# Kernel tuning notes

Hardware: AMD Instinct MI355X
Metric: run time of the kernel (lower is better)

Reference implementation:

```python
import jax, jax.numpy as jnp
import numpy as np

N = 100000          # nodes
E = 1600000         # edges (avg degree 16)
D_IN = 128
D_OUT = 128
K = 3               # Chebyshev order
LAMBDA_MAX = 2.0    # PyG default for sym normalization


def setup_inputs() -> dict:
    key = jax.random.key(0)
    k1, k2, k3, k4 = jax.random.split(key, 4)
    x = jax.random.normal(k1, (N, D_IN), dtype=jnp.float32)
    edge_index = jax.random.randint(k2, (2, E), 0, N, dtype=jnp.int32)
    # Glorot-ish init for the K per-order linear weights
    weight = jax.random.normal(k3, (K, D_IN, D_OUT), dtype=jnp.float32) * (1.0 / np.sqrt(D_IN))
    bias = jax.random.normal(k4, (D_OUT,), dtype=jnp.float32) * 0.01
    return {"x": x, "edge_index": edge_index, "weight": weight, "bias": bias}


def reference(x, edge_index, weight, bias):
    src, dst = edge_index[0], edge_index[1]
    n = x.shape[0]

    # remove self loops (zero their weight), symmetric normalization
    ew = jnp.where(src != dst, 1.0, 0.0).astype(x.dtype)
    deg = jax.ops.segment_sum(ew, src, num_segments=n)
    dis = jnp.where(deg > 0, jax.lax.rsqrt(jnp.maximum(deg, 1.0)), 0.0)
    norm = dis[src] * ew * dis[dst]          # D^-1/2 A D^-1/2 entries

    # scaled Laplacian T-hat = (2/lmax) L - I, L = I - A_norm
    off_w = -(2.0 / LAMBDA_MAX) * norm       # off-diagonal entries
    diag_w = 2.0 / LAMBDA_MAX - 1.0          # = 0 for lambda_max=2

    def spmm(h):  # T-hat @ h : gather-multiply-scatter over edges
        agg = jax.ops.segment_sum(off_w[:, None] * h[src], dst, num_segments=n)
        return agg + diag_w * h

    # Chebyshev recurrence: Tx_k = 2 T-hat Tx_{k-1} - Tx_{k-2}
    Tx0 = x
    out = Tx0 @ weight[0]
    Tx1 = spmm(Tx0)
    out = out + Tx1 @ weight[1]
    for k in range(2, weight.shape[0]):
        Tx2 = 2.0 * spmm(Tx1) - Tx0
        out = out + Tx2 @ weight[k]
        Tx0, Tx1 = Tx1, Tx2
    return out + bias
```

## Files before the change

### kernel.cpp

```cpp
#include <hip/hip_runtime.h>
#include <hip/hip_bf16.h>

typedef __hip_bfloat16 bf16;
typedef __attribute__((ext_vector_type(8))) short short8;
typedef __attribute__((ext_vector_type(4))) float float4v;
typedef __attribute__((ext_vector_type(2))) float float2v;

#define N_NODES 100000
#define M_PAD   100096
#define N_EDGES 1600000
#define D 128
#define K_CAT 384
#define BUCKET_CAP 56
#define NBIN 392
#define BIN_CAP 4608
#define CHUNK 4096
#define NCHUNK 391
#define PREPB 192

__device__ __forceinline__ bf16 f2b(float v) { return __float2bfloat16(v); }
__device__ __forceinline__ float ub(unsigned int u, int k) {
    return (float)((u >> (k * 8)) & 0xffu);
}
__device__ __forceinline__ float2v cvt2lo(unsigned int u) {
    float a, b;
    asm("v_cvt_f32_ubyte0 %0, %2\n\t"
        "v_cvt_f32_ubyte1 %1, %2"
        : "=&v"(a), "=&v"(b) : "v"(u));
    float2v o; o.x = a; o.y = b; return o;
}
__device__ __forceinline__ float2v cvt2hi(unsigned int u) {
    float a, b;
    asm("v_cvt_f32_ubyte2 %0, %2\n\t"
        "v_cvt_f32_ubyte3 %1, %2"
        : "=&v"(a), "=&v"(b) : "v"(u));
    float2v o; o.x = a; o.y = b; return o;
}

__global__ __launch_bounds__(256) void phaseA_prep_kernel(const int* __restrict__ src,
                                                          const int* __restrict__ dst,
                                                          const float* __restrict__ w,
                                                          const float* __restrict__ bias,
                                                          int* __restrict__ gCursD,
                                                          int* __restrict__ gCursS,
                                                          unsigned int* __restrict__ gBinD,
                                                          unsigned char* __restrict__ gBinS,
                                                          bf16* __restrict__ wT,
                                                          float* __restrict__ biasf) {
    __shared__ int histD[NBIN], histS[NBIN], cursD[NBIN], cursS[NBIN];
    int tid = threadIdx.x;
    if (blockIdx.x >= NCHUNK) {
        int i = (blockIdx.x - NCHUNK) * 256 + tid;
        int o = i / K_CAT, k = i % K_CAT;
        float v;
        if (k < 128) {
            v = w[k * D + o] - w[2 * 16384 + k * D + o];
        } else if (k < 256) {
            v = w[16384 + (k - 128) * D + o];
        } else {
            v = 2.0f * w[2 * 16384 + (k - 256) * D + o];
        }
        wT[i] = f2b(v);
        if (i < D) biasf[i] = bias[i];
        return;
    }
    for (int t = tid; t < NBIN; t += 256) { histD[t] = 0; histS[t] = 0; }
    __syncthreads();
    int e0 = blockIdx.x * CHUNK;
    for (int i = tid; i < CHUNK; i += 256) {
        int e = e0 + i;
        if (e >= N_EDGES) break;
        int s = src[e], d = dst[e];
        if (s == d) continue;
        atomicAdd(&histD[d >> 8], 1);
        atomicAdd(&histS[s >> 8], 1);
    }
    __syncthreads();
    for (int t = tid; t < NBIN; t += 256) {
        cursD[t] = (histD[t] > 0) ? atomicAdd(&gCursD[t], histD[t]) : 0;
        cursS[t] = (histS[t] > 0) ? atomicAdd(&gCursS[t], histS[t]) : 0;
    }
    __syncthreads();
    for (int i = tid; i < CHUNK; i += 256) {
        int e = e0 + i;
        if (e >= N_EDGES) break;
        int s = src[e], d = dst[e];
        if (s == d) continue;
        int bd = d >> 8, bs = s >> 8;
        int sd = atomicAdd(&cursD[bd], 1);
        if (sd < BIN_CAP) gBinD[(size_t)bd * BIN_CAP + sd] = ((unsigned int)s << 8) | (unsigned int)(d & 255);
        int ss = atomicAdd(&cursS[bs], 1);
        if (ss < BIN_CAP) gBinS[(size_t)bs * BIN_CAP + ss] = (unsigned char)(s & 255);
    }
}

__global__ __launch_bounds__(256) void phaseBq_kernel(const int* __restrict__ gCursD,
                                                      const int* __restrict__ gCursS,
                                                      const unsigned int* __restrict__ gBinD,
                                                      const unsigned char* __restrict__ gBinS,
                                                      const float* __restrict__ x,
                                                      int* __restrict__ cnt,
                                                      float* __restrict__ dis,
                                                      int* __restrict__ bucket,
                                                      unsigned char* __restrict__ xq,
                                                      float* __restrict__ xscale,
                                                      float* __restrict__ dsx0) {
    __shared__ int curs[256];
    int tid = threadIdx.x;
    int b = blockIdx.x;
    curs[tid] = 0;
    __syncthreads();
    if (b < NBIN) {
        int count = min(gCursD[b], BIN_CAP);
        const unsigned int* rec = gBinD + (size_t)b * BIN_CAP;
        int n0 = b << 8;
        for (int j = tid; j < count; j += 256) {
            unsigned int r = rec[j];
            int dloc = r & 255;
            int s = (int)(r >> 8);
            int slot = atomicAdd(&curs[dloc], 1);
            if (slot < BUCKET_CAP) bucket[(size_t)(n0 + dloc) * BUCKET_CAP + slot] = s;
        }
        __syncthreads();
        int n = n0 + tid;
        if (n < N_NODES) cnt[n] = curs[tid];
    } else {
        int bb = b - NBIN;
        int count = min(gCursS[bb], BIN_CAP);
        const unsigned char* rec = gBinS + (size_t)bb * BIN_CAP;
        for (int j = tid; j < count; j += 256) {
            atomicAdd(&curs[rec[j]], 1);
        }
        __syncthreads();
        int n0 = bb << 8;
        int n = n0 + tid;
        if (n < N_NODES) {
            int c = curs[tid];
            dis[n] = (c > 0) ? rsqrtf((float)c) : 0.0f;
        }
        int wv = tid >> 6, lane = tid & 63;
        for (int i = 0; i < 64; i++) {
            int nn = n0 + wv * 64 + i;
            if (nn >= N_NODES) break;
            float2 v = *(const float2*)(x + (size_t)nn * D + lane * 2);
            float m = fmaxf(fabsf(v.x), fabsf(v.y));
#pragma unroll
            for (int k = 1; k < 64; k <<= 1) m = fmaxf(m, __shfl_xor(m, k));
            float inv = (m > 0.0f) ? 127.0f / m : 0.0f;
            int q0 = (int)rintf(v.x * inv) + 128;
            int q1 = (int)rintf(v.y * inv) + 128;
            *(unsigned short*)(xq + (size_t)nn * D + lane * 2) =
                (unsigned short)((q0 & 0xff) | ((q1 & 0xff) << 8));
            if (lane == 0) {
                float sc = m * (1.0f / 127.0f);
                int cc = curs[wv * 64 + i];
                float dnn = (cc > 0) ? rsqrtf((float)cc) : 0.0f;
                xscale[nn] = sc;
                dsx0[nn] = dnn * sc;
            }
        }
    }
}

template<int OUTQ>
__global__ __launch_bounds__(256) void spmm_q_kernel(const unsigned char* __restrict__ hq,
                                                     const float* __restrict__ dsx,
                                                     const float* __restrict__ dis,
                                                     const int* __restrict__ cnt,
                                                     const int* __restrict__ bucket,
                                                     unsigned char* __restrict__ outq,
                                                     float* __restrict__ oscale,
                                                     float* __restrict__ odsx,
                                                     bf16* __restrict__ outb) {
    int wv = threadIdx.x >> 6;
    int lane = threadIdx.x & 63;
    int n = blockIdx.x * 4 + wv;
    int c = min(cnt[n], BUCKET_CAP);
    float dn = dis[n];
    int q = lane >> 4;
    int r = lane & 15;
    int s_l = 0;
    float w_l = 0.0f;
    if (lane < c) {
        s_l = bucket[(size_t)n * BUCKET_CAP + lane];
        w_l = -dsx[s_l] * dn;
    }
    const unsigned char* hr = hq + (r << 3);

    float2v acc2[4];
#pragma unroll
    for (int k = 0; k < 4; k++) acc2[k] = (float2v)0.0f;
    float cw = 0.0f;

    int sA = __shfl(s_l, q), sB = __shfl(s_l, 4 + q);
    float wA = __shfl(w_l, q), wB = __shfl(w_l, 4 + q);
    uint2 uA = *(const uint2*)(hr + (size_t)sA * D);
    uint2 uB = *(const uint2*)(hr + (size_t)sB * D);

    for (int j0 = 0; j0 < c; j0 += 8) {
        int nj = j0 + 8;
        int sA2 = __shfl(s_l, nj + q);
        int sB2 = __shfl(s_l, nj + 4 + q);
        float wA2 = __shfl(w_l, nj + q);
        float wB2 = __shfl(w_l, nj + 4 + q);
        uint2 uA2 = *(const uint2*)(hr + (size_t)sA2 * D);
        uint2 uB2 = *(const uint2*)(hr + (size_t)sB2 * D);
        cw += wA + wB;
        float2v wAv; wAv.x = wA; wAv.y = wA;
        float2v wBv; wBv.x = wB; wBv.y = wB;
        acc2[0] += wAv * cvt2lo(uA.x);
        acc2[1] += wAv * cvt2hi(uA.x);
        acc2[2] += wAv * cvt2lo(uA.y);
        acc2[3] += wAv * cvt2hi(uA.y);
        acc2[0] += wBv * cvt2lo(uB.x);
        acc2[1] += wBv * cvt2hi(uB.x);
        acc2[2] += wBv * cvt2lo(uB.y);
        acc2[3] += wBv * cvt2hi(uB.y);
        sA = sA2; sB = sB2; wA = wA2; wB = wB2; uA = uA2; uB = uB2;
    }

    float acc[8];
#pragma unroll
    for (int k = 0; k < 4; k++) { acc[2 * k] = acc2[k].x; acc[2 * k + 1] = acc2[k].y; }
#pragma unroll
    for (int k = 0; k < 8; k++) {
        acc[k] += __shfl_xor(acc[k], 16);
        acc[k] += __shfl_xor(acc[k], 32);
    }
    cw += __shfl_xor(cw, 16);
    cw += __shfl_xor(cw, 32);
#pragma unroll
    for (int k = 0; k < 8; k++) acc[k] -= 128.0f * cw;

    if (OUTQ) {
        float m = 0.0f;
#pragma unroll
        for (int k = 0; k < 8; k++) m = fmaxf(m, fabsf(acc[k]));
#pragma unroll
        for (int k = 1; k < 16; k <<= 1) m = fmaxf(m, __shfl_xor(m, k));
        float inv = (m > 0.0f) ? 127.0f / m : 0.0f;
        if (q == 0) {
            unsigned int b0 = 0, b1 = 0;
#pragma unroll
            for (int k = 0; k < 4; k++)
                b0 |= ((unsigned int)((int)rintf(acc[k] * inv) + 128) & 0xffu) << (8 * k);
#pragma unroll
            for (int k = 0; k < 4; k++)
                b1 |= ((unsigned int)((int)rintf(acc[4 + k] * inv) + 128) & 0xffu) << (8 * k);
            uint2 pk; pk.x = b0; pk.y = b1;
            *(uint2*)(outq + (size_t)n * D + (r << 3)) = pk;
            if (lane == 0) {
                float sc = m * (1.0f / 127.0f);
                oscale[n] = sc;
                odsx[n] = dn * sc;
            }
        }
    } else {
        if (q == 0) {
            unsigned int p0 = (unsigned int)__bfloat16_as_ushort(f2b(acc[0])) |
                              ((unsigned int)__bfloat16_as_ushort(f2b(acc[1])) << 16);
            unsigned int p1 = (unsigned int)__bfloat16_as_ushort(f2b(acc[2])) |
                              ((unsigned int)__bfloat16_as_ushort(f2b(acc[3])) << 16);
            unsigned int p2 = (unsigned int)__bfloat16_as_ushort(f2b(acc[4])) |
                              ((unsigned int)__bfloat16_as_ushort(f2b(acc[5])) << 16);
            unsigned int p3 = (unsigned int)__bfloat16_as_ushort(f2b(acc[6])) |
                              ((unsigned int)__bfloat16_as_ushort(f2b(acc[7])) << 16);
            uint4 pk; pk.x = p0; pk.y = p1; pk.z = p2; pk.w = p3;
            *(uint4*)(outb + (size_t)n * D + (r << 3)) = pk;
        }
    }
}

#define AS_STRIDE 40
__device__ __forceinline__ void stage_q8(bf16* __restrict__ As,
                                         const unsigned char* __restrict__ srcq,
                                         const float* __restrict__ scl,
                                         int nb, int kb) {
    int tid = threadIdx.x;
#pragma unroll
    for (int t = 0; t < 2; t++) {
        int c = tid + t * 256;
        int row = c >> 2;
        int off = (c & 3) * 8;
        int gr = nb + row;
        if (gr > N_NODES - 1) gr = N_NODES - 1;
        uint2 u = *(const uint2*)(srcq + (size_t)gr * D + kb + off);
        float sc = scl[gr];
        float f0 = sc * (ub(u.x, 0) - 128.0f);
        float f1 = sc * (ub(u.x, 1) - 128.0f);
        float f2 = sc * (ub(u.x, 2) - 128.0f);
        float f3 = sc * (ub(u.x, 3) - 128.0f);
        float f4 = sc * (ub(u.y, 0) - 128.0f);
        float f5 = sc * (ub(u.y, 1) - 128.0f);
        float f6 = sc * (ub(u.y, 2) - 128.0f);
        float f7 = sc * (ub(u.y, 3) - 128.0f);
        uint4 pk;
        pk.x = (unsigned int)__bfloat16_as_ushort(f2b(f0)) |
               ((unsigned int)__bfloat16_as_ushort(f2b(f1)) << 16);
        pk.y = (unsigned int)__bfloat16_as_ushort(f2b(f2)) |
               ((unsigned int)__bfloat16_as_ushort(f2b(f3)) << 16);
        pk.z = (unsigned int)__bfloat16_as_ushort(f2b(f4)) |
               ((unsigned int)__bfloat16_as_ushort(f2b(f5)) << 16);
        pk.w = (unsigned int)__bfloat16_as_ushort(f2b(f6)) |
               ((unsigned int)__bfloat16_as_ushort(f2b(f7)) << 16);
        *(uint4*)(As + row * AS_STRIDE + off) = pk;
    }
}

__global__ __launch_bounds__(256) void gemm_kernel(const unsigned char* __restrict__ xq,
                                                   const float* __restrict__ xscale,
                                                   const unsigned char* __restrict__ tx1q,
                                                   const float* __restrict__ tx1scale,
                                                   const bf16* __restrict__ agg2,
                                                   const bf16* __restrict__ wT,
                                                   const float* __restrict__ biasf,
                                                   float* __restrict__ out) {
    __shared__ bf16 As[128 * AS_STRIDE];
    __shared__ bf16 Bs[128 * AS_STRIDE];

    int tid = threadIdx.x;
    int nb = blockIdx.x * 128;
    int w = tid >> 6;
    int lane = tid & 63;
    int lq = lane >> 4;
    int lr = lane & 15;

    float4v acc[2][8];
#pragma unroll
    for (int i = 0; i < 2; i++)
#pragma unroll
        for (int j = 0; j < 8; j++) acc[i][j] = (float4v)0.0f;

    for (int kc = 0; kc < 12; kc++) {
        int kbase = kc * 32;
        if (kc < 4) {
            stage_q8(As, xq, xscale, nb, kc * 32);
        } else if (kc < 8) {
            stage_q8(As, tx1q, tx1scale, nb, (kc - 4) * 32);
        } else {
            int soff = (kc & 3) * 32;
#pragma unroll
            for (int t = 0; t < 2; t++) {
                int c = tid + t * 256;
                int row = c >> 2;
                int off = (c & 3) * 8;
                uint4 v = *(const uint4*)(agg2 + (size_t)(nb + row) * D + soff + off);
                *(uint4*)(As + row * AS_STRIDE + off) = v;
            }
        }
#pragma unroll
        for (int t = 0; t < 2; t++) {
            int c = tid + t * 256;
            int row = c >> 2;
            int off = (c & 3) * 8;
            uint4 v = *(const uint4*)(wT + (size_t)row * K_CAT + kbase + off);
            *(uint4*)(Bs + row * AS_STRIDE + off) = v;
        }
        __syncthreads();

        short8 af[2], bfr[8];
#pragma unroll
        for (int i = 0; i < 2; i++)
            af[i] = *(const short8*)(As + (w * 32 + i * 16 + lr) * AS_STRIDE + lq * 8);
#pragma unroll
        for (int j = 0; j < 8; j++)
            bfr[j] = *(const short8*)(Bs + (j * 16 + lr) * AS_STRIDE + lq * 8);
#pragma unroll
        for (int i = 0; i < 2; i++)
#pragma unroll
            for (int j = 0; j < 8; j++)
                acc[i][j] = __builtin_amdgcn_mfma_f32_16x16x32_bf16(af[i], bfr[j], acc[i][j], 0, 0, 0);
        __syncthreads();
    }

#pragma unroll
    for (int i = 0; i < 2; i++) {
        int rowb = nb + w * 32 + i * 16 + lq * 4;
#pragma unroll
        for (int j = 0; j < 8; j++) {
            int col = j * 16 + lr;
            float bv = biasf[col];
#pragma unroll
            for (int r = 0; r < 4; r++) {
                int row = rowb + r;
                if (row < N_NODES) out[(size_t)row * D + col] = acc[i][j][r] + bv;
            }
        }
    }
}

extern "C" void kernel_launch(void* const* d_in, const int* in_sizes, int n_in,
                              void* d_out, int out_size, void* d_ws, size_t ws_size,
                              hipStream_t stream) {
    const float* x    = (const float*)d_in[0];
    const int*   ei   = (const int*)d_in[1];
    const float* w    = (const float*)d_in[2];
    const float* bias = (const float*)d_in[3];
    float* out = (float*)d_out;

    char* p = (char*)d_ws;
    int*   cnt      = (int*)p;     p += (size_t)N_NODES * 4;
    float* dis      = (float*)p;   p += (size_t)N_NODES * 4;
    int*   gCurs    = (int*)p;     p += (size_t)2 * NBIN * 4;
    float* dsx0     = (float*)p;   p += (size_t)M_PAD * 4;
    float* xscale   = (float*)p;   p += (size_t)M_PAD * 4;
    float* tx1scale = (float*)p;   p += (size_t)M_PAD * 4;
    float* dsx1     = (float*)p;   p += (size_t)M_PAD * 4;
    int*   bucket   = (int*)p;     p += (size_t)N_NODES * BUCKET_CAP * 4;
    char*  buf1     = p;           p += (size_t)M_PAD * D;
    unsigned char* xq = (unsigned char*)p; p += (size_t)M_PAD * D;
    bf16*  agg2     = (bf16*)p;    p += (size_t)M_PAD * D * 2;
    bf16*  wT       = (bf16*)p;    p += (size_t)D * K_CAT * 2;
    float* biasf    = (float*)p;   p += (size_t)D * 4;

    int*   gCursD = gCurs;
    int*   gCursS = gCurs + NBIN;
    unsigned int*  gBinD = (unsigned int*)buf1;
    unsigned char* gBinS = (unsigned char*)(gBinD + (size_t)NBIN * BIN_CAP);
    unsigned char* tx1q  = (unsigned char*)buf1;

    hipMemsetAsync(gCurs, 0, (size_t)2 * NBIN * 4, stream);

    phaseA_prep_kernel<<<NCHUNK + PREPB, 256, 0, stream>>>(ei, ei + N_EDGES, w, bias,
                                                           gCursD, gCursS, gBinD, gBinS,
                                                           wT, biasf);
    phaseBq_kernel<<<2 * NBIN, 256, 0, stream>>>(gCursD, gCursS, gBinD, gBinS, x,
                                                 cnt, dis, bucket, xq, xscale, dsx0);
    spmm_q_kernel<1><<<N_NODES / 4, 256, 0, stream>>>(xq, dsx0, dis, cnt, bucket,
                                                      tx1q, tx1scale, dsx1, (bf16*)nullptr);
    spmm_q_kernel<0><<<N_NODES / 4, 256, 0, stream>>>(tx1q, dsx1, dis, cnt, bucket,
                                                      (unsigned char*)nullptr, (float*)nullptr,
                                                      (float*)nullptr, agg2);
    gemm_kernel<<<M_PAD / 128, 256, 0, stream>>>(xq, xscale, tx1q, tx1scale,
                                                 agg2, wT, biasf, out);
}
```

Before: 353.4 us.

## Move x quantization into prep kernel and use persistent grid for SpMM

Quantizing x to int8 now happens in 25000 extra blocks of the first prep kernel, one wave per node. Before, it ran as a serial 64-node loop per wave inside the second half of phaseB, which had only 392 blocks. phaseB now only computes degrees and combines them with the precomputed scale. The SpMM kernels switch to a fixed grid of 2048 blocks that loop over node groups. This aims to raise parallelism in the quantization step and to cut block launch overhead in SpMM, at the cost of a much larger first grid and possible load imbalance across the grid-stride loop.

```diff
diff --git a/kernel.cpp b/kernel.cpp
--- a/kernel.cpp
+++ b/kernel.cpp
@@ -17,6 +17,8 @@
 #define CHUNK 4096
 #define NCHUNK 391
 #define PREPB 192
+#define QUANTB 25000
+#define SPMM_GRID 2048
 
 __device__ __forceinline__ bf16 f2b(float v) { return __float2bfloat16(v); }
 __device__ __forceinline__ float ub(unsigned int u, int k) {
@@ -37,18 +39,32 @@
     float2v o; o.x = a; o.y = b; return o;
 }
 
-__global__ __launch_bounds__(256) void phaseA_prep_kernel(const int* __restrict__ src,
-                                                          const int* __restrict__ dst,
-                                                          const float* __restrict__ w,
-                                                          const float* __restrict__ bias,
-                                                          int* __restrict__ gCursD,
-                                                          int* __restrict__ gCursS,
-                                                          unsigned int* __restrict__ gBinD,
-                                                          unsigned char* __restrict__ gBinS,
-                                                          bf16* __restrict__ wT,
-                                                          float* __restrict__ biasf) {
+__global__ __launch_bounds__(256) void phaseA_prep_quant_kernel(
+        const int* __restrict__ src, const int* __restrict__ dst,
+        const float* __restrict__ w, const float* __restrict__ bias,
+        const float* __restrict__ x,
+        int* __restrict__ gCursD, int* __restrict__ gCursS,
+        unsigned int* __restrict__ gBinD, unsigned char* __restrict__ gBinS,
+        bf16* __restrict__ wT, float* __restrict__ biasf,
+        unsigned char* __restrict__ xq, float* __restrict__ xscale) {
     __shared__ int histD[NBIN], histS[NBIN], cursD[NBIN], cursS[NBIN];
     int tid = threadIdx.x;
+    if (blockIdx.x >= NCHUNK + PREPB) {
+        int i = blockIdx.x - (NCHUNK + PREPB);
+        int wv = tid >> 6, lane = tid & 63;
+        int n = i * 4 + wv;
+        float2 v = *(const float2*)(x + (size_t)n * D + lane * 2);
+        float m = fmaxf(fabsf(v.x), fabsf(v.y));
+#pragma unroll
+        for (int k = 1; k < 64; k <<= 1) m = fmaxf(m, __shfl_xor(m, k));
+        float inv = (m > 0.0f) ? 127.0f / m : 0.0f;
+        int q0 = (int)rintf(v.x * inv) + 128;
+        int q1 = (int)rintf(v.y * inv) + 128;
+        *(unsigned short*)(xq + (size_t)n * D + lane * 2) =
+            (unsigned short)((q0 & 0xff) | ((q1 & 0xff) << 8));
+        if (lane == 0) xscale[n] = m * (1.0f / 127.0f);
+        return;
+    }
     if (blockIdx.x >= NCHUNK) {
         int i = (blockIdx.x - NCHUNK) * 256 + tid;
         int o = i / K_CAT, k = i % K_CAT;
@@ -94,17 +110,15 @@
     }
 }
 
-__global__ __launch_bounds__(256) void phaseBq_kernel(const int* __restrict__ gCursD,
-                                                      const int* __restrict__ gCursS,
-                                                      const unsigned int* __restrict__ gBinD,
-                                                      const unsigned char* __restrict__ gBinS,
-                                                      const float* __restrict__ x,
-                                                      int* __restrict__ cnt,
-                                                      float* __restrict__ dis,
-                                                      int* __restrict__ bucket,
-                                                      unsigned char* __restrict__ xq,
-                                                      float* __restrict__ xscale,
-                                                      float* __restrict__ dsx0) {
+__global__ __launch_bounds__(256) void phaseB_kernel(const int* __restrict__ gCursD,
+                                                     const int* __restrict__ gCursS,
+                                                     const unsigned int* __restrict__ gBinD,
+                                                     const unsigned char* __restrict__ gBinS,
+                                                     const float* __restrict__ xscale,
+                                                     int* __restrict__ cnt,
+                                                     float* __restrict__ dis,
+                                                     int* __restrict__ bucket,
+                                                     float* __restrict__ dsx0) {
     __shared__ int curs[256];
     int tid = threadIdx.x;
     int b = blockIdx.x;
@@ -132,49 +146,28 @@
             atomicAdd(&curs[rec[j]], 1);
         }
         __syncthreads();
-        int n0 = bb << 8;
-        int n = n0 + tid;
+        int n = (bb << 8) + tid;
         if (n < N_NODES) {
             int c = curs[tid];
-            dis[n] = (c > 0) ? rsqrtf((float)c) : 0.0f;
-        }
-        int wv = tid >> 6, lane = tid & 63;
-        for (int i = 0; i < 64; i++) {
-            int nn = n0 + wv * 64 + i;
-            if (nn >= N_NODES) break;
-            float2 v = *(const float2*)(x + (size_t)nn * D + lane * 2);
-            float m = fmaxf(fabsf(v.x), fabsf(v.y));
-#pragma unroll
-            for (int k = 1; k < 64; k <<= 1) m = fmaxf(m, __shfl_xor(m, k));
-            float inv = (m > 0.0f) ? 127.0f / m : 0.0f;
-            int q0 = (int)rintf(v.x * inv) + 128;
-            int q1 = (int)rintf(v.y * inv) + 128;
-            *(unsigned short*)(xq + (size_t)nn * D + lane * 2) =
-                (unsigned short)((q0 & 0xff) | ((q1 & 0xff) << 8));
-            if (lane == 0) {
-                float sc = m * (1.0f / 127.0f);
-                int cc = curs[wv * 64 + i];
-                float dnn = (cc > 0) ? rsqrtf((float)cc) : 0.0f;
-                xscale[nn] = sc;
-                dsx0[nn] = dnn * sc;
-            }
+            float dn = (c > 0) ? rsqrtf((float)c) : 0.0f;
+            dis[n] = dn;
+            dsx0[n] = dn * xscale[n];
         }
     }
 }
 
 template<int OUTQ>
-__global__ __launch_bounds__(256) void spmm_q_kernel(const unsigned char* __restrict__ hq,
-                                                     const float* __restrict__ dsx,
-                                                     const float* __restrict__ dis,
-                                                     const int* __restrict__ cnt,
-                                                     const int* __restrict__ bucket,
-                                                     unsigned char* __restrict__ outq,
-                                                     float* __restrict__ oscale,
-                                                     float* __restrict__ odsx,
-                                                     bf16* __restrict__ outb) {
-    int wv = threadIdx.x >> 6;
+__device__ __forceinline__ void spmm_body(int n,
+                                          const unsigned char* __restrict__ hq,
+                                          const float* __restrict__ dsx,
+                                          const float* __restrict__ dis,
+                                          const int* __restrict__ cnt,
+                                          const int* __restrict__ bucket,
+                                          unsigned char* __restrict__ outq,
+                                          float* __restrict__ oscale,
+                                          float* __restrict__ odsx,
+                                          bf16* __restrict__ outb) {
     int lane = threadIdx.x & 63;
-    int n = blockIdx.x * 4 + wv;
     int c = min(cnt[n], BUCKET_CAP);
     float dn = dis[n];
     int q = lane >> 4;
@@ -269,6 +262,21 @@
             *(uint4*)(outb + (size_t)n * D + (r << 3)) = pk;
         }
     }
+}
+
+template<int OUTQ>
+__global__ __launch_bounds__(256) void spmm_q_kernel(const unsigned char* __restrict__ hq,
+                                                     const float* __restrict__ dsx,
+                                                     const float* __restrict__ dis,
+                                                     const int* __restrict__ cnt,
+                                                     const int* __restrict__ bucket,
+                                                     unsigned char* __restrict__ outq,
+                                                     float* __restrict__ oscale,
+                                                     float* __restrict__ odsx,
+                                                     bf16* __restrict__ outb) {
+    int wv = threadIdx.x >> 6;
+    for (int g = blockIdx.x; g < N_NODES / 4; g += gridDim.x)
+        spmm_body<OUTQ>(g * 4 + wv, hq, dsx, dis, cnt, bucket, outq, oscale, odsx, outb);
 }
 
 #define AS_STRIDE 40
@@ -421,16 +429,16 @@
 
     hipMemsetAsync(gCurs, 0, (size_t)2 * NBIN * 4, stream);
 
-    phaseA_prep_kernel<<<NCHUNK + PREPB, 256, 0, stream>>>(ei, ei + N_EDGES, w, bias,
-                                                           gCursD, gCursS, gBinD, gBinS,
-                                                           wT, biasf);
-    phaseBq_kernel<<<2 * NBIN, 256, 0, stream>>>(gCursD, gCursS, gBinD, gBinS, x,
-                                                 cnt, dis, bucket, xq, xscale, dsx0);
-    spmm_q_kernel<1><<<N_NODES / 4, 256, 0, stream>>>(xq, dsx0, dis, cnt, bucket,
-                                                      tx1q, tx1scale, dsx1, (bf16*)nullptr);
-    spmm_q_kernel<0><<<N_NODES / 4, 256, 0, stream>>>(tx1q, dsx1, dis, cnt, bucket,
-                                                      (unsigned char*)nullptr, (float*)nullptr,
-                                                      (float*)nullptr, agg2);
+    phaseA_prep_quant_kernel<<<NCHUNK + PREPB + QUANTB, 256, 0, stream>>>(
+        ei, ei + N_EDGES, w, bias, x,
+        gCursD, gCursS, gBinD, gBinS, wT, biasf, xq, xscale);
+    phaseB_kernel<<<2 * NBIN, 256, 0, stream>>>(gCursD, gCursS, gBinD, gBinS, xscale,
+                                                cnt, dis, bucket, dsx0);
+    spmm_q_kernel<1><<<SPMM_GRID, 256, 0, stream>>>(xq, dsx0, dis, cnt, bucket,
+                                                    tx1q, tx1scale, dsx1, (bf16*)nullptr);
+    spmm_q_kernel<0><<<SPMM_GRID, 256, 0, stream>>>(tx1q, dsx1, dis, cnt, bucket,
+                                                    (unsigned char*)nullptr, (float*)nullptr,
+                                                    (float*)nullptr, agg2);
     gemm_kernel<<<M_PAD / 128, 256, 0, stream>>>(xq, xscale, tx1q, tx1scale,
                                                  agg2, wT, biasf, out);
 }
```

New measurement: 316.8 us, median of 2. 10.4% less time.
